# Performance work log

Hardware: AMD Instinct MI355X
Metric: run time of the kernel (lower is better)

Reference implementation:

```python
import jax, jax.numpy as jnp
import numpy as np

N = 65536          # pixels
F = 224            # spectral bands (num_features)
P = 6              # num_endmembers
H = 256            # hidden_dim


def setup_inputs() -> dict:
    key = jax.random.key(0)
    ks = jax.random.split(key, 8)
    s = lambda fan_in: 1.0 / np.sqrt(fan_in)
    return {
        "abundance_matrix": jax.random.normal(ks[0], (N, P), jnp.float32),
        "Y": jax.random.normal(ks[1], (N, F), jnp.float32),
        "W1": jax.random.normal(ks[2], (F, H), jnp.float32) * s(F),
        "b1": jnp.zeros((H,), jnp.float32),
        "W2": jax.random.normal(ks[3], (H, H), jnp.float32) * s(H),
        "b2": jnp.zeros((H,), jnp.float32),
        "W3": jax.random.normal(ks[4], (H, F), jnp.float32) * s(H),
        "b3": jnp.zeros((F,), jnp.float32),
    }


def reference(abundance_matrix, Y, W1, b1, W2, b2, W3, b3):
    # MLP is pointwise over pixels, so apply once to all pixels [N,F] -> [N,F]
    h = jax.nn.relu(Y @ W1 + b1)
    h = jax.nn.relu(h @ W2 + b2)
    logits = h @ W3 + b3                      # [N, F]

    cls = jnp.argmax(abundance_matrix, axis=-1)          # [N]
    masks = cls[None, :] == jnp.arange(P)[:, None]       # [P, N]

    # Masked per-class softmax over the pixel axis (per feature column).
    neg = jnp.finfo(logits.dtype).min
    masked_logits = jnp.where(masks[:, :, None], logits[None], neg)  # [P, N, F]
    w = jax.nn.softmax(masked_logits, axis=1)                        # [P, N, F]
    w = w * masks[:, :, None]                                        # exact zeros off-class

    M = jnp.einsum('pnf,nf->pf', w, Y)                   # [P, F] endmembers
    counts = masks.sum(axis=1)                           # [P]
    M = jnp.where((counts > 0)[:, None], M, jnp.zeros_like(M))

    Y_hat = abundance_matrix @ M                         # [N, F]
    return Y_hat
```

## Files before the change

kernel.cpp:

```cpp
#include <hip/hip_runtime.h>
#include <stdint.h>

typedef short s16x8 __attribute__((ext_vector_type(8)));
typedef short s16x4 __attribute__((ext_vector_type(4)));
typedef float f32x4 __attribute__((ext_vector_type(4)));

#define NPIX 65536
#define FEAT 224
#define PEND 6
#define HID  256

__device__ __forceinline__ unsigned short f2bf(float x) {
  unsigned u = __float_as_uint(x);
  return (unsigned short)((u + 0x7FFFu + ((u >> 16) & 1u)) >> 16);
}
__device__ __forceinline__ float bf2f(unsigned short b) {
  return __uint_as_float(((unsigned)b) << 16);
}
__device__ __forceinline__ void glds16(const void* g, void* l) {
  __builtin_amdgcn_global_load_lds(
      (const __attribute__((address_space(1))) unsigned int*)g,
      (__attribute__((address_space(3))) unsigned int*)l, 16, 0, 0);
}

__global__ void cvtW_all(const float* __restrict__ W1, const float* __restrict__ W2,
                         const float* __restrict__ W3,
                         unsigned short* __restrict__ W1t, unsigned short* __restrict__ W2t,
                         unsigned short* __restrict__ W3t, float* __restrict__ gz) {
  int i = blockIdx.x * 256 + threadIdx.x;
  if (i < 57344) {
    int n = i / 224, k = i - n * 224;
    W1t[i] = f2bf(W1[k * 256 + n]);
  } else if (i < 122880) {
    int i2 = i - 57344;
    int n = i2 >> 8, k = i2 & 255;
    W2t[i2] = f2bf(W2[k * 256 + n]);
  } else if (i < 188416) {
    int i3 = i - 122880;
    int n = i3 >> 8, k = i3 & 255;
    W3t[i3] = (n < FEAT) ? f2bf(W3[k * FEAT + n]) : (unsigned short)0;
  } else if (i < 191104) {
    gz[i - 188416] = 0.f;
  }
}

__global__ __launch_bounds__(256, 3)
void fused_mlp(const float* __restrict__ Y,
               const unsigned short* __restrict__ W1t,
               const unsigned short* __restrict__ W2t,
               const unsigned short* __restrict__ W3t,
               const float* __restrict__ b1, const float* __restrict__ b2,
               const float* __restrict__ b3, const float* __restrict__ ab,
               float* __restrict__ gsum, float* __restrict__ gsumY) {
  __shared__ __align__(16) unsigned short hS[64 * 256];
  __shared__ __align__(16) unsigned short Bs[2][8192];
  __shared__ __align__(16) unsigned short clsS[64];
  unsigned short* AsB = hS;
  float* redE = (float*)hS;
  float* redY = redE + PEND * FEAT;

  const int tid = threadIdx.x;
  const int wid = tid >> 6, lane = tid & 63;
  const int mrow = lane & 15, quad = lane >> 4;
  const int brow = lane >> 2, bk8 = (lane & 3) * 8;
  const int arow = tid >> 2, aqtr = tid & 3;
  const long row0 = (long)blockIdx.x * 64;

  f32x4 acc[4][4];
  float4 pv0, pv1;

#define STAGE_W(s) do {                                                     \
    const unsigned short* Wp_; int ld_, k0_;                                \
    if ((s) < 7)       { Wp_ = W1t; ld_ = 224; k0_ = (s) * 32; }            \
    else if ((s) < 15) { Wp_ = W2t; ld_ = 256; k0_ = ((s) - 7) * 32; }      \
    else               { Wp_ = W3t; ld_ = 256; k0_ = ((s) - 15) * 32; }     \
    unsigned short* dst_ = &Bs[(s) & 1][wid * 2048];                        \
    _Pragma("unroll")                                                       \
    for (int c_ = 0; c_ < 4; c_++)                                          \
      glds16(Wp_ + (size_t)(wid * 64 + c_ * 16 + brow) * ld_ + k0_ + bk8,   \
             dst_ + c_ * 512);                                              \
  } while (0)

#define LOADA(p) do {                                                       \
    const float* s_ = Y + (row0 + arow) * FEAT + (p) * 32 + aqtr * 8;       \
    pv0 = *(const float4*)s_; pv1 = *(const float4*)(s_ + 4);               \
  } while (0)

#define WRITEA(p) do {                                                      \
    unsigned short* d_ = AsB + ((p) & 1) * 2304 + arow * 36 + aqtr * 8;     \
    s16x4 lo_ = {(short)f2bf(pv0.x), (short)f2bf(pv0.y),                    \
                 (short)f2bf(pv0.z), (short)f2bf(pv0.w)};                   \
    s16x4 hi_ = {(short)f2bf(pv1.x), (short)f2bf(pv1.y),                    \
                 (short)f2bf(pv1.z), (short)f2bf(pv1.w)};                   \
    *(s16x4*)d_ = lo_; *(s16x4*)(d_ + 4) = hi_;                             \
  } while (0)

#define LOAD_B(buf)                                                         \
    _Pragma("unroll")                                                       \
    for (int j = 0; j < 4; j++)                                             \
      bfv[j] = *(const s16x8*)(&Bs[buf][(wid * 64 + j * 16 + mrow) * 32 + quad * 8]);

#define MFMA_ALL()                                                          \
    _Pragma("unroll")                                                       \
    for (int i = 0; i < 4; i++)                                             \
      _Pragma("unroll")                                                     \
      for (int j = 0; j < 4; j++)                                           \
        acc[i][j] = __builtin_amdgcn_mfma_f32_16x16x32_bf16(af[i], bfv[j], acc[i][j], 0, 0, 0);

#define ZERO_ACC()                                                          \
    _Pragma("unroll")                                                       \
    for (int i = 0; i < 4; i++)                                             \
      _Pragma("unroll")                                                     \
      for (int j = 0; j < 4; j++) acc[i][j] = {0.f, 0.f, 0.f, 0.f};

  ZERO_ACC();
  LOADA(0); STAGE_W(0); WRITEA(0);
  __syncthreads();
  for (int p = 0; p < 7; p++) {
    if (p < 6) { LOADA(p + 1); STAGE_W(p + 1); }
    else       { STAGE_W(7); }
    s16x8 af[4], bfv[4];
    const unsigned short* Ab = AsB + (p & 1) * 2304;
#pragma unroll
    for (int i = 0; i < 4; i++) {
      const unsigned short* pa = Ab + (i * 16 + mrow) * 36 + quad * 8;
      s16x4 lo = *(const s16x4*)pa, hi = *(const s16x4*)(pa + 4);
      af[i] = __builtin_shufflevector(lo, hi, 0, 1, 2, 3, 4, 5, 6, 7);
    }
    LOAD_B(p & 1);
    MFMA_ALL();
    if (p < 6) WRITEA(p + 1);
    __syncthreads();
  }
#pragma unroll
  for (int j = 0; j < 4; j++) {
    int col = wid * 64 + j * 16 + mrow;
    float bb = b1[col];
    int cs = col >> 3, c7 = col & 7;
#pragma unroll
    for (int i = 0; i < 4; i++) {
#pragma unroll
      for (int r = 0; r < 4; r++) {
        int row = i * 16 + quad * 4 + r;
        hS[row * 256 + ((cs ^ (row & 7)) << 3) + c7] = f2bf(fmaxf(acc[i][j][r] + bb, 0.f));
      }
    }
  }
  __syncthreads();

  ZERO_ACC();
  for (int p = 0; p < 8; p++) {
    STAGE_W(p < 7 ? 8 + p : 15);
    const int k0 = p * 32, buf = (7 + p) & 1;
    s16x8 af[4], bfv[4];
#pragma unroll
    for (int i = 0; i < 4; i++) {
      int R = i * 16 + mrow;
      int ch = (k0 >> 3) + quad;
      af[i] = *(const s16x8*)(hS + R * 256 + ((ch ^ (R & 7)) << 3));
    }
    LOAD_B(buf);
    MFMA_ALL();
    __syncthreads();
  }
#pragma unroll
  for (int j = 0; j < 4; j++) {
    int col = wid * 64 + j * 16 + mrow;
    float bb = b2[col];
    int cs = col >> 3, c7 = col & 7;
#pragma unroll
    for (int i = 0; i < 4; i++) {
#pragma unroll
      for (int r = 0; r < 4; r++) {
        int row = i * 16 + quad * 4 + r;
        hS[row * 256 + ((cs ^ (row & 7)) << 3) + c7] = f2bf(fmaxf(acc[i][j][r] + bb, 0.f));
      }
    }
  }
  __syncthreads();

  ZERO_ACC();
  for (int p = 0; p < 8; p++) {
    if (p < 7) STAGE_W(16 + p);
    const int k0 = p * 32, buf = (15 + p) & 1;
    s16x8 af[4], bfv[4];
#pragma unroll
    for (int i = 0; i < 4; i++) {
      int R = i * 16 + mrow;
      int ch = (k0 >> 3) + quad;
      af[i] = *(const s16x8*)(hS + R * 256 + ((ch ^ (R & 7)) << 3));
    }
    LOAD_B(buf);
    MFMA_ALL();
    __syncthreads();
  }
#pragma unroll
  for (int j = 0; j < 4; j++) {
    int col = wid * 64 + j * 16 + mrow;
    if (col < FEAT) {
      float bb = b3[col];
      int cs = col >> 3, c7 = col & 7;
#pragma unroll
      for (int i = 0; i < 4; i++) {
#pragma unroll
        for (int r = 0; r < 4; r++) {
          int row = i * 16 + quad * 4 + r;
          hS[row * 256 + ((cs ^ (row & 7)) << 3) + c7] = f2bf(__expf(acc[i][j][r] + bb));
        }
      }
    }
  }
  if (tid < 64) {
    const float* a = ab + (row0 + tid) * PEND;
    float best = a[0]; int c = 0;
#pragma unroll
    for (int p = 1; p < PEND; p++) { float v = a[p]; if (v > best) { best = v; c = p; } }
    clsS[tid] = (unsigned short)c;
  }
  __syncthreads();

  const bool act = lane < 56;
  const int f0 = lane * 4;
  float accE[PEND][4], accY[PEND][4];
#pragma unroll
  for (int p = 0; p < PEND; p++)
#pragma unroll
    for (int i = 0; i < 4; i++) { accE[p][i] = 0.f; accY[p][i] = 0.f; }

#pragma unroll 4
  for (int r = wid; r < 64; r += 4) {
    int c = __builtin_amdgcn_readfirstlane((int)clsS[r]);
    if (act) {
      const unsigned short* pe = hS + r * 256 + (((f0 >> 3) ^ (r & 7)) << 3) + (f0 & 7);
      ushort4 e4 = *(const ushort4*)pe;
      float4 y4 = *(const float4*)(Y + (row0 + r) * FEAT + f0);
      float e[4] = {bf2f(e4.x), bf2f(e4.y), bf2f(e4.z), bf2f(e4.w)};
      float ey[4] = {e[0] * y4.x, e[1] * y4.y, e[2] * y4.z, e[3] * y4.w};
#define RK_CASE(P)                                                               \
      case P:                                                                    \
        _Pragma("unroll")                                                        \
        for (int i = 0; i < 4; i++) { accE[P][i] += e[i]; accY[P][i] += ey[i]; } \
        break;
      switch (c) {
        RK_CASE(0) RK_CASE(1) RK_CASE(2) RK_CASE(3) RK_CASE(4) RK_CASE(5)
      }
#undef RK_CASE
    }
  }
  __syncthreads();

  for (int w = 0; w < 4; w++) {
    if (wid == w && act) {
#pragma unroll
      for (int p = 0; p < PEND; p++) {
        float4* pe = (float4*)(redE + p * FEAT + f0);
        float4* py = (float4*)(redY + p * FEAT + f0);
        float4 ve = {accE[p][0], accE[p][1], accE[p][2], accE[p][3]};
        float4 vy = {accY[p][0], accY[p][1], accY[p][2], accY[p][3]};
        if (w == 0) { *pe = ve; *py = vy; }
        else {
          float4 oe = *pe, oy = *py;
          oe.x += ve.x; oe.y += ve.y; oe.z += ve.z; oe.w += ve.w;
          oy.x += vy.x; oy.y += vy.y; oy.z += vy.z; oy.w += vy.w;
          *pe = oe; *py = oy;
        }
      }
    }
    __syncthreads();
  }

  for (int i = tid; i < PEND * FEAT; i += 256) {
    atomicAdd(&gsum[i], redE[i]);
    atomicAdd(&gsumY[i], redY[i]);
  }
#undef STAGE_W
#undef LOADA
#undef WRITEA
#undef LOAD_B
#undef MFMA_ALL
#undef ZERO_ACC
}

__global__ __launch_bounds__(256)
void yhat(const float* __restrict__ ab, const float* __restrict__ gsum,
          const float* __restrict__ gsumY, float* __restrict__ out) {
  constexpr int ROWS = 64;
  __shared__ float Ms[PEND * FEAT];
  __shared__ float aS[ROWS * PEND];
  const int tid = threadIdx.x;
  for (int i = tid; i < PEND * FEAT; i += 256) {
    float s = gsum[i];
    Ms[i] = (s > 0.f) ? gsumY[i] / s : 0.f;
  }
  const long n0 = (long)blockIdx.x * ROWS;
  for (int i = tid; i < ROWS * PEND; i += 256) aS[i] = ab[n0 * PEND + i];
  __syncthreads();

  const int wid = tid >> 6;
  const int lane = tid & 63;
  if (lane >= 56) return;
  const int f0 = lane * 4;
  float4 Mr[PEND];
#pragma unroll
  for (int p = 0; p < PEND; p++) Mr[p] = *(const float4*)(Ms + p * FEAT + f0);

  for (int r = wid; r < ROWS; r += 4) {
    float a[PEND];
#pragma unroll
    for (int p = 0; p < PEND; p++) a[p] = aS[r * PEND + p];
    float4 o = {0.f, 0.f, 0.f, 0.f};
#pragma unroll
    for (int p = 0; p < PEND; p++) {
      o.x += a[p] * Mr[p].x; o.y += a[p] * Mr[p].y;
      o.z += a[p] * Mr[p].z; o.w += a[p] * Mr[p].w;
    }
    *(float4*)(out + (n0 + r) * FEAT + f0) = o;
  }
}

extern "C" void kernel_launch(void* const* d_in, const int* in_sizes, int n_in,
                              void* d_out, int out_size, void* d_ws, size_t ws_size,
                              hipStream_t stream) {
  const float* ab = (const float*)d_in[0];
  const float* Y  = (const float*)d_in[1];
  const float* W1 = (const float*)d_in[2];
  const float* b1 = (const float*)d_in[3];
  const float* W2 = (const float*)d_in[4];
  const float* b2 = (const float*)d_in[5];
  const float* W3 = (const float*)d_in[6];
  const float* b3 = (const float*)d_in[7];
  float* out = (float*)d_out;

  char* ws = (char*)d_ws;
  const size_t oW1t  = 0;
  const size_t oW2t  = 114688;
  const size_t oW3t  = 245760;
  const size_t osum  = 376832;

  unsigned short* W1t = (unsigned short*)(ws + oW1t);
  unsigned short* W2t = (unsigned short*)(ws + oW2t);
  unsigned short* W3t = (unsigned short*)(ws + oW3t);
  float* gsum  = (float*)(ws + osum);
  float* gsumY = (float*)(ws + osum + 5376);

  cvtW_all<<<747, 256, 0, stream>>>(W1, W2, W3, W1t, W2t, W3t, gsum);
  fused_mlp<<<1024, 256, 0, stream>>>(Y, W1t, W2t, W3t, b1, b2, b3, ab, gsum, gsumY);
  yhat<<<1024, 256, 0, stream>>>(ab, gsum, gsumY, out);
}
```

Before: 206.4 us.

## Spread global atomics over slots and finalize endmembers in last block

Each block now adds its per-class partial sums into one of up to 16 slot copies instead of a single shared buffer. This is meant to cut atomic contention, since 1024 blocks all hit the same 2688 addresses. A done-counter lets the last finishing block reduce the slots and write the final M = sumY/sumE, so yhat now only copies M instead of dividing in every block. The cost is a larger zeroing pass, a threadfence and counter atomic per block, and a serial tail reduction run by a single block.

```diff
diff --git a/kernel.cpp b/kernel.cpp
--- a/kernel.cpp
+++ b/kernel.cpp
@@ -9,6 +9,7 @@
 #define FEAT 224
 #define PEND 6
 #define HID  256
+#define MSZ  (PEND * FEAT)
 
 __device__ __forceinline__ unsigned short f2bf(float x) {
   unsigned u = __float_as_uint(x);
@@ -26,7 +27,8 @@
 __global__ void cvtW_all(const float* __restrict__ W1, const float* __restrict__ W2,
                          const float* __restrict__ W3,
                          unsigned short* __restrict__ W1t, unsigned short* __restrict__ W2t,
-                         unsigned short* __restrict__ W3t, float* __restrict__ gz) {
+                         unsigned short* __restrict__ W3t,
+                         float* __restrict__ part, unsigned* __restrict__ done, int nslot) {
   int i = blockIdx.x * 256 + threadIdx.x;
   if (i < 57344) {
     int n = i / 224, k = i - n * 224;
@@ -39,8 +41,11 @@
     int i3 = i - 122880;
     int n = i3 >> 8, k = i3 & 255;
     W3t[i3] = (n < FEAT) ? f2bf(W3[k * FEAT + n]) : (unsigned short)0;
-  } else if (i < 191104) {
-    gz[i - 188416] = 0.f;
+  } else {
+    int z = i - 188416;
+    int nz = 2 * nslot * MSZ;
+    if (z < nz) part[z] = 0.f;
+    else if (z == nz) *done = 0u;
   }
 }
 
@@ -51,13 +56,14 @@
                const unsigned short* __restrict__ W3t,
                const float* __restrict__ b1, const float* __restrict__ b2,
                const float* __restrict__ b3, const float* __restrict__ ab,
-               float* __restrict__ gsum, float* __restrict__ gsumY) {
+               float* __restrict__ part, float* __restrict__ Mout,
+               unsigned* __restrict__ done, int nslot) {
   __shared__ __align__(16) unsigned short hS[64 * 256];
   __shared__ __align__(16) unsigned short Bs[2][8192];
   __shared__ __align__(16) unsigned short clsS[64];
   unsigned short* AsB = hS;
   float* redE = (float*)hS;
-  float* redY = redE + PEND * FEAT;
+  float* redY = redE + MSZ;
 
   const int tid = threadIdx.x;
   const int wid = tid >> 6, lane = tid & 63;
@@ -269,9 +275,36 @@
     __syncthreads();
   }
 
-  for (int i = tid; i < PEND * FEAT; i += 256) {
-    atomicAdd(&gsum[i], redE[i]);
-    atomicAdd(&gsumY[i], redY[i]);
+  {
+    const int slot = blockIdx.x & (nslot - 1);
+    float* gE = part + (size_t)slot * MSZ;
+    float* gY = part + (size_t)nslot * MSZ + (size_t)slot * MSZ;
+    for (int i = tid; i < MSZ; i += 256) {
+      atomicAdd(&gE[i], redE[i]);
+      atomicAdd(&gY[i], redY[i]);
+    }
+  }
+  __threadfence();
+  __syncthreads();
+  if (tid == 0) {
+    unsigned t = atomicAdd(done, 1u);
+    clsS[0] = (t == gridDim.x - 1) ? (unsigned short)1 : (unsigned short)0;
+  }
+  __syncthreads();
+  if (clsS[0]) {
+    __threadfence();
+    const float* pE = part;
+    const float* pY = part + (size_t)nslot * MSZ;
+    for (int i = tid; i < MSZ; i += 256) {
+      float se = 0.f, sy = 0.f;
+      for (int s = 0; s < nslot; s++) {
+        se += __hip_atomic_load(&pE[(size_t)s * MSZ + i], __ATOMIC_RELAXED,
+                                __HIP_MEMORY_SCOPE_AGENT);
+        sy += __hip_atomic_load(&pY[(size_t)s * MSZ + i], __ATOMIC_RELAXED,
+                                __HIP_MEMORY_SCOPE_AGENT);
+      }
+      Mout[i] = (se > 0.f) ? sy / se : 0.f;
+    }
   }
 #undef STAGE_W
 #undef LOADA
@@ -282,16 +315,13 @@
 }
 
 __global__ __launch_bounds__(256)
-void yhat(const float* __restrict__ ab, const float* __restrict__ gsum,
-          const float* __restrict__ gsumY, float* __restrict__ out) {
+void yhat(const float* __restrict__ ab, const float* __restrict__ M,
+          float* __restrict__ out) {
   constexpr int ROWS = 64;
-  __shared__ float Ms[PEND * FEAT];
+  __shared__ float Ms[MSZ];
   __shared__ float aS[ROWS * PEND];
   const int tid = threadIdx.x;
-  for (int i = tid; i < PEND * FEAT; i += 256) {
-    float s = gsum[i];
-    Ms[i] = (s > 0.f) ? gsumY[i] / s : 0.f;
-  }
+  for (int i = tid; i < MSZ; i += 256) Ms[i] = M[i];
   const long n0 = (long)blockIdx.x * ROWS;
   for (int i = tid; i < ROWS * PEND; i += 256) aS[i] = ab[n0 * PEND + i];
   __syncthreads();
@@ -332,18 +362,30 @@
   float* out = (float*)d_out;
 
   char* ws = (char*)d_ws;
-  const size_t oW1t  = 0;
-  const size_t oW2t  = 114688;
-  const size_t oW3t  = 245760;
-  const size_t osum  = 376832;
+  const size_t oW1t = 0;
+  const size_t oW2t = 114688;
+  const size_t oW3t = 245760;
+  const size_t opart = 376832;
+
+  int nslot = 16;
+  while (nslot > 1 &&
+         opart + (size_t)2 * nslot * MSZ * 4 + MSZ * 4 + 64 > ws_size)
+    nslot >>= 1;
+  const size_t oM    = opart + (size_t)2 * nslot * MSZ * 4;
+  const size_t odone = oM + MSZ * 4;
 
   unsigned short* W1t = (unsigned short*)(ws + oW1t);
   unsigned short* W2t = (unsigned short*)(ws + oW2t);
   unsigned short* W3t = (unsigned short*)(ws + oW3t);
-  float* gsum  = (float*)(ws + osum);
-  float* gsumY = (float*)(ws + osum + 5376);
-
-  cvtW_all<<<747, 256, 0, stream>>>(W1, W2, W3, W1t, W2t, W3t, gsum);
-  fused_mlp<<<1024, 256, 0, stream>>>(Y, W1t, W2t, W3t, b1, b2, b3, ab, gsum, gsumY);
-  yhat<<<1024, 256, 0, stream>>>(ab, gsum, gsumY, out);
-}
+  float* part = (float*)(ws + opart);
+  float* M    = (float*)(ws + oM);
+  unsigned* done = (unsigned*)(ws + odone);
+
+  const int cvt_threads = 188416 + 2 * nslot * MSZ + 1;
+  const int cvt_blocks = (cvt_threads + 255) / 256;
+
+  cvtW_all<<<cvt_blocks, 256, 0, stream>>>(W1, W2, W3, W1t, W2t, W3t, part, done, nslot);
+  fused_mlp<<<1024, 256, 0, stream>>>(Y, W1t, W2t, W3t, b1, b2, b3, ab,
+                                      part, M, done, nslot);
+  yhat<<<1024, 256, 0, stream>>>(ab, M, out);
+}
```

Result: slower. 295.1 us (+43.0%).
